# Performance work log

Measured on AMD Instinct MI355X. Metric: run time of the kernel, lower is better.

## Reference

```python
import jax, jax.numpy as jnp
import numpy as np

MAX_DEGREE = 8
N_COEFF = 45  # sum of (2l+1) for l = 0,2,...,8
N_DIRS = 90
BATCH = 50000
N_SHELLS = 4
OUT_SIZE = 4


def _make_ls(max_degree, n_coeff):
    ls = np.zeros(n_coeff, dtype=np.int32)
    for l in range(0, max_degree + 1, 2):
        for m in range(-l, l + 1):
            ls[int(0.5 * l * (l + 1) + m)] = l
    return ls

LS = _make_ls(MAX_DEGREE, N_COEFF)
SCALE = np.sqrt(np.pi / (2.0 * LS + 1.0)).astype(np.float32)  # [K]
LS_IDX = (LS // 2).astype(np.int32)  # [K], index into degree axis of weights


def setup_inputs() -> dict:
    key = jax.random.key(0)
    ks = jax.random.split(key, 10)
    inp = {
        'x': jax.random.normal(ks[0], (BATCH, N_SHELLS, N_COEFF), dtype=jnp.float32),
        'sft': jax.random.normal(ks[1], (N_COEFF, N_DIRS), dtype=jnp.float32),
        'isft': jax.random.normal(ks[2], (N_DIRS, N_COEFF), dtype=jnp.float32),
        'w1': jax.random.uniform(ks[3], (16, N_SHELLS, MAX_DEGREE // 2 + 1), dtype=jnp.float32),
        'w2': jax.random.uniform(ks[4], (32, 16, MAX_DEGREE // 2 + 1), dtype=jnp.float32),
        'w3': jax.random.uniform(ks[5], (64, 32, MAX_DEGREE // 2 + 1), dtype=jnp.float32),
        'w4': jax.random.uniform(ks[6], (32, 64, MAX_DEGREE // 2 + 1), dtype=jnp.float32),
        'w5': jax.random.uniform(ks[7], (16, 32, MAX_DEGREE // 2 + 1), dtype=jnp.float32),
        'w6': jax.random.uniform(ks[8], (4, 16, MAX_DEGREE // 2 + 1), dtype=jnp.float32),
    }
    return inp


def _sconv(x, w, ls_idx, scale):
    # x: [B, C_in, K]; w: [C_out, C_in, L/2+1]
    w_exp = w[:, :, ls_idx]  # [C_out, C_in, K]
    # out[b,o,k] = scale[k] * sum_c w_exp[o,c,k] * x[b,c,k]
    return jnp.einsum('bck,ock->bok', x, w_exp) * scale[None, None, :]


def _nonlinearity(x, sft, isft):
    # x: [B, C, K] -> signal space [B, C, P] -> relu -> back to SH space
    sig = jnp.einsum('pk,bck->bcp', isft, x)
    return jnp.einsum('kp,bcp->bck', sft, jax.nn.relu(sig))


def reference(x, sft, isft, w1, w2, w3, w4, w5, w6):
    ls_idx = jnp.asarray(LS_IDX)
    scale = jnp.asarray(SCALE)
    for w in (w1, w2, w3, w4, w5, w6):
        x = _sconv(x, w, ls_idx, scale)
        x = _nonlinearity(x, sft, isft)
    return jnp.squeeze(x)
```

## Files before the change

kernel.cpp:

```cpp
#include <hip/hip_runtime.h>

#define NT 512

typedef __attribute__((ext_vector_type(8)))  short bh8;
typedef __attribute__((ext_vector_type(16))) float f16v;
typedef __attribute__((ext_vector_type(4)))  float f4v;

#define FW_H    0
#define FW_L    28672
#define W2A32_H 57344
#define W2A32_L 61952
#define W3B_H   66560
#define W3B_L   71168

#define YHo  0
#define S2o  3072
#define XHo  9216
#define NU   12672

__device__ __forceinline__ unsigned short f2bf(float f) {
  unsigned u = __float_as_uint(f);
  return (unsigned short)((u + 0x7fffu + ((u >> 16) & 1u)) >> 16);
}
__device__ __forceinline__ float bf2f(unsigned short h) {
  return __uint_as_float(((unsigned)h) << 16);
}
__device__ __forceinline__ int lidxf(int k) {
  return (k < 1) ? 0 : (k < 6) ? 1 : (k < 15) ? 2 : (k < 28) ? 3 : 4;
}
__device__ __forceinline__ float scale_from_j(int j) {
  float s = 1.7724539f;
  s = (j == 1) ? 0.79266548f : s;
  s = (j == 2) ? 0.59081795f : s;
  s = (j == 3) ? 0.49159026f : s;
  s = (j >= 4) ? 0.42988324f : s;
  return s;
}
__device__ __forceinline__ float rcp_from_j(int j) {
  float s = 0.56418958f;
  s = (j == 1) ? 1.2615663f : s;
  s = (j == 2) ? 1.6925688f : s;
  s = (j == 3) ? 2.0342144f : s;
  s = (j >= 4) ? 2.3262120f : s;
  return s;
}
__device__ __forceinline__ unsigned rne_adj(float v) {
  const unsigned u = __float_as_uint(v);
  return u + 0x7fffu + ((u >> 16) & 1u);
}
__device__ __forceinline__ void store4h(unsigned short* dh,
                                        float v0, float v1, float v2, float v3) {
  const unsigned a0 = rne_adj(v0), a1 = rne_adj(v1);
  const unsigned a2 = rne_adj(v2), a3 = rne_adj(v3);
  *(uint2*)dh = make_uint2(__builtin_amdgcn_perm(a1, a0, 0x07060302u),
                           __builtin_amdgcn_perm(a3, a2, 0x07060302u));
}

__global__ void scnn_prep(const float* __restrict__ sft, const float* __restrict__ isft,
                          const float* __restrict__ w1, const float* __restrict__ w2,
                          const float* __restrict__ w3, const float* __restrict__ w4,
                          const float* __restrict__ w5, const float* __restrict__ w6,
                          unsigned short* __restrict__ wsu) {
  const int gid = blockIdx.x * NT + threadIdx.x;
  const int gstr = gridDim.x * NT;
  const float* wp[6] = {w1, w2, w3, w4, w5, w6};
  const int CIN[6] = {4, 16, 32, 64, 32, 16};
  const int COUT[6] = {16, 32, 64, 32, 16, 4};
  const int LG[6] = {3, 4, 5, 6, 5, 4};
  const int NST[6] = {2, 3, 5, 10, 5, 3};
  const int NTC[6] = {1, 2, 4, 2, 1, 1};
  const int FOFF[6] = {0, 2, 8, 28, 48, 53};
#pragma unroll
  for (int l = 0; l < 6; ++l) {
    const int cin = CIN[l], cout = COUT[l], lg = LG[l], cinP = 1 << lg;
    const int nst = NST[l];
    const int n = NTC[l] * nst * 512;
    const float* w = wp[l];
    const int base = FOFF[l] * 512;
    for (int i = gid; i < n; i += gstr) {
      const int fid = i >> 9, lane = (i >> 3) & 63, e = i & 7;
      const int nt = fid / nst, st = fid - nt * nst;
      const int o = nt * 16 + (lane & 15);
      const int s = st * 32 + (lane >> 4) * 8 + e;
      const int j = s >> lg, c = s & (cinP - 1);
      float v = 0.f;
      if (o < cout && j < 5 && c < cin) v = w[(o * cin + c) * 5 + j];
      const unsigned short h = f2bf(v);
      wsu[FW_H + base + i] = h;
      wsu[FW_L + base + i] = f2bf(v - bf2f(h));
    }
  }
  for (int i = gid; i < 9 * 512; i += gstr) {
    const int fid = i >> 9, lane = (i >> 3) & 63, e = i & 7;
    const int mt = fid / 3, ks = fid - mt * 3;
    const int p = mt * 32 + (lane & 31);
    const int k = ks * 16 + (lane >> 5) * 8 + e;
    const float v = (p < 90 && k < 45) ? isft[p * 45 + k] : 0.f;
    const unsigned short h = f2bf(v);
    wsu[W2A32_H + i] = h;
    wsu[W2A32_L + i] = f2bf(v - bf2f(h));
  }
  for (int i = gid; i < 9 * 512; i += gstr) {
    const int fid = i >> 9, lane = (i >> 3) & 63, e = i & 7;
    const int ntK = fid / 3, sl = fid - ntK * 3;
    const int kk = ntK * 16 + (lane & 15);
    const int p = sl * 32 + (lane >> 4) * 8 + e;
    float v = 0.f;
    if (kk < 45 && p < 90) v = sft[kk * 90 + p] * scale_from_j(lidxf(kk));
    const unsigned short h = f2bf(v);
    wsu[W3B_H + i] = h;
    wsu[W3B_L + i] = f2bf(v - bf2f(h));
  }
}

__device__ __forceinline__ f16v s2tile_pre(const unsigned short* U,
                                           const unsigned short* fh, int nt, int lof,
                                           bh8 pah) {
  f16v a;
#pragma unroll
  for (int e = 0; e < 16; ++e) a[e] = 0.f;
  const unsigned short* yb = U + YHo + nt * 3 * 512 + lof;
  {
    const bh8 bhv = *(const bh8*)&yb[0];
    a = __builtin_amdgcn_mfma_f32_32x32x16_bf16(pah, bhv, a, 0, 0, 0);
  }
#pragma unroll
  for (int ks = 1; ks < 3; ++ks) {
    const bh8 ah = *(const bh8*)&fh[ks * 512];
    const bh8 bhv = *(const bh8*)&yb[ks * 512];
    a = __builtin_amdgcn_mfma_f32_32x32x16_bf16(ah, bhv, a, 0, 0, 0);
  }
  return a;
}
__device__ __forceinline__ void writes_s(unsigned short* U, f16v acc, int mt,
                                         int nt, int llo, int lhi) {
  const int so = S2o + ((nt * 2 + (llo >> 4)) * 3 + mt) * 512 + (llo & 15) * 8 + lhi * 4;
#pragma unroll
  for (int g = 0; g < 4; ++g) {
    store4h(&U[so + g * 128],
            fmaxf(acc[g * 4 + 0], 0.f), fmaxf(acc[g * 4 + 1], 0.f),
            fmaxf(acc[g * 4 + 2], 0.f), fmaxf(acc[g * 4 + 3], 0.f));
  }
}

template <int layer, int mt>
__device__ __forceinline__ void atile(unsigned short* U,
                                      const unsigned short* __restrict__ wsu,
                                      int nt, int l15, int q4, int lof) {
  constexpr int lg   = (layer == 0) ? 3 : (layer == 1) ? 4 : (layer == 2) ? 5
                     : (layer == 3) ? 6 : (layer == 4) ? 5 : 4;
  constexpr int cinP = 1 << lg;
  constexpr int NSTc = (layer == 0) ? 2 : (layer == 1) ? 3 : (layer == 2) ? 5
                     : (layer == 3) ? 10 : (layer == 4) ? 5 : 3;
  constexpr int FOFFc= (layer == 0) ? 0 : (layer == 1) ? 2 : (layer == 2) ? 8
                     : (layer == 3) ? 28 : (layer == 4) ? 48 : 53;
  constexpr int hi5 = (5 * cinP + 31) >> 5;
  constexpr int hi4 = (4 * cinP + 31) >> 5;
  constexpr int lo3 = (3 * cinP) >> 5;
  constexpr int lo4 = cinP >> 3;
  constexpr int lo = (mt == 0) ? 0 : (mt == 1) ? lo3 : lo4;
  constexpr int hi = (mt == 0) ? hi4 : hi5;
  (void)cinP;

  const int k = mt * 16 + l15;
  const int jb = lidxf(k) << lg;
  const unsigned short* wfh = wsu + FW_H + (FOFFc + nt * NSTc) * 512 + lof;
  f4v a;
  a[0] = a[1] = a[2] = a[3] = 0.f;
#pragma unroll
  for (int st = lo; st < hi; ++st) {
    const int S = st * 32 + q4 * 8;
    const unsigned c0 = (unsigned)(S - jb);
    const unsigned cc = c0 < 64u ? c0 : 64u;
    const bh8 xh = *(const bh8*)&U[XHo + k * 72 + (int)cc];
    const bh8 wh = *(const bh8*)&wfh[st * 512];
    a = __builtin_amdgcn_mfma_f32_16x16x32_bf16(xh, wh, a, 0, 0, 0);
  }
  const int off = (((nt >> 1) * 3 + mt) << 9) +
                  ((q4 >> 1) * 32 + (nt & 1) * 16 + l15) * 8 + (q4 & 1) * 4;
  store4h(&U[YHo + off], a[0], a[1], a[2], a[3]);
}

__device__ __forceinline__ void dstore(unsigned short* U, f4v a, int ntK, int mtO,
                                       int l15, int q4, int layer_zero_mode) {
  const int kk = ntK * 16 + l15;
  const int oc = mtO * 16 + q4 * 4;
  store4h(&U[XHo + kk * 72 + oc], a[0], a[1], a[2], a[3]);
  if (layer_zero_mode == 1) {
    *(uint2*)&U[XHo + kk * 72 + oc + 32] = make_uint2(0u, 0u);
  }
  if (layer_zero_mode == 2) {
    *(uint2*)&U[XHo + kk * 72 + oc + 16] = make_uint2(0u, 0u);
  }
}

template <int layer>
__device__ __forceinline__ void layer_body(unsigned short* U,
                                           const unsigned short* __restrict__ wsu,
                                           int tid, int wv, int llo, int lhi,
                                           int l15, int q4, int lof) {
  constexpr int nt16 = (layer == 2) ? 4 : (layer == 1 || layer == 3) ? 2 : 1;
  constexpr int n32  = (layer == 2) ? 2 : 1;
  constexpr int zmode = (layer == 3) ? 1 : (layer == 4) ? 2 : 0;

  {
    constexpr int T = 3 * nt16;
    for (int t = wv; t < T; t += 8) {
      const int mt = t % 3, nt = t / 3;
      if (mt == 0)      atile<layer, 0>(U, wsu, nt, l15, q4, lof);
      else if (mt == 1) atile<layer, 1>(U, wsu, nt, l15, q4, lof);
      else              atile<layer, 2>(U, wsu, nt, l15, q4, lof);
    }
  }
  constexpr int T2 = 3 * n32;
  const bool hA = wv < T2;
  const unsigned short* fh = wsu + W2A32_H + (wv % 3) * 3 * 512 + lof;
  bh8 pah;
  if (hA) pah = *(const bh8*)&fh[0];
  __syncthreads();

  {
    f16v a0;
    if (hA) a0 = s2tile_pre(U, fh, wv / 3, lof, pah);
    if (hA) writes_s(U, a0, wv % 3, wv / 3, llo, lhi);
  }
  const int grp = wv >> 2, mtO = wv & 3;
  const bool hD = mtO < nt16;
  const int ntKa = (grp == 0) ? 0 : 2;
  const unsigned short* fba = wsu + W3B_H + ntKa * 3 * 512 + lof;
  bh8 pb;
  if (hD) pb = *(const bh8*)&fba[0];
  __syncthreads();

  if (hD) {
    const unsigned short* ab = U + S2o + mtO * 3 * 512 + lof;
    if (grp == 0) {
      const unsigned short* fbb = wsu + W3B_H + 3 * 512 + lof;
      f4v a0, a1;
      a0[0] = a0[1] = a0[2] = a0[3] = 0.f;
      a1[0] = a1[1] = a1[2] = a1[3] = 0.f;
#pragma unroll
      for (int sl = 0; sl < 3; ++sl) {
        const bh8 ah = *(const bh8*)&ab[sl * 512];
        bh8 b0h;
        if (sl == 0) b0h = pb;
        else         b0h = *(const bh8*)&fba[sl * 512];
        const bh8 b1h = *(const bh8*)&fbb[sl * 512];
        a0 = __builtin_amdgcn_mfma_f32_16x16x32_bf16(ah, b0h, a0, 0, 0, 0);
        a1 = __builtin_amdgcn_mfma_f32_16x16x32_bf16(ah, b1h, a1, 0, 0, 0);
      }
      dstore(U, a0, 0, mtO, l15, q4, zmode);
      dstore(U, a1, 1, mtO, l15, q4, zmode);
    } else {
      f4v a;
      a[0] = a[1] = a[2] = a[3] = 0.f;
#pragma unroll
      for (int sl = 0; sl < 3; ++sl) {
        const bh8 ah = *(const bh8*)&ab[sl * 512];
        bh8 bh_;
        if (sl == 0) bh_ = pb;
        else         bh_ = *(const bh8*)&fba[sl * 512];
        a = __builtin_amdgcn_mfma_f32_16x16x32_bf16(ah, bh_, a, 0, 0, 0);
      }
      dstore(U, a, 2, mtO, l15, q4, zmode);
    }
  }
  __syncthreads();
}

__global__ __launch_bounds__(NT, 8)
void scnn_main(const float* __restrict__ xin, const unsigned short* __restrict__ wsu,
               float* __restrict__ out) {
  __shared__ __align__(16) unsigned short U[NU];
  const int tid = threadIdx.x, b = blockIdx.x;
  const int lane = tid & 63, wv = tid >> 6;
  const int llo = lane & 31, lhi = lane >> 5;
  const int l15 = lane & 15, q4 = lane >> 4;
  const int lof = lane << 3;

  for (int i = tid; i < 864; i += NT)
    ((uint2*)&U[XHo])[i] = make_uint2(0u, 0u);
  __syncthreads();
  for (int i = tid; i < 180; i += NT) {
    const int c = i / 45, k = i - c * 45;
    const float v = xin[(size_t)b * 180 + i] * scale_from_j(lidxf(k));
    U[XHo + k * 72 + c] = f2bf(v);
  }
  __syncthreads();

  layer_body<0>(U, wsu, tid, wv, llo, lhi, l15, q4, lof);
  layer_body<1>(U, wsu, tid, wv, llo, lhi, l15, q4, lof);
  layer_body<2>(U, wsu, tid, wv, llo, lhi, l15, q4, lof);
  layer_body<3>(U, wsu, tid, wv, llo, lhi, l15, q4, lof);
  layer_body<4>(U, wsu, tid, wv, llo, lhi, l15, q4, lof);
  layer_body<5>(U, wsu, tid, wv, llo, lhi, l15, q4, lof);

  for (int i = tid; i < 180; i += NT) {
    const int c = i / 45, k = i - c * 45;
    const float v = bf2f(U[XHo + k * 72 + c]);
    out[(size_t)b * 180 + i] = v * rcp_from_j(lidxf(k));
  }
}

extern "C" void kernel_launch(void* const* d_in, const int* in_sizes, int n_in,
                              void* d_out, int out_size, void* d_ws, size_t ws_size,
                              hipStream_t stream) {
  (void)n_in; (void)out_size; (void)ws_size;
  const float* x    = (const float*)d_in[0];
  const float* sft  = (const float*)d_in[1];
  const float* isft = (const float*)d_in[2];
  const float* w1   = (const float*)d_in[3];
  const float* w2   = (const float*)d_in[4];
  const float* w3   = (const float*)d_in[5];
  const float* w4   = (const float*)d_in[6];
  const float* w5   = (const float*)d_in[7];
  const float* w6   = (const float*)d_in[8];
  float* out = (float*)d_out;
  unsigned short* wsu = (unsigned short*)d_ws;
  const int nb = in_sizes[0] / 180;
  scnn_prep<<<64, NT, 0, stream>>>(sft, isft, w1, w2, w3, w4, w5, w6, wsu);
  scnn_main<<<nb, NT, 0, stream>>>(x, wsu, out);
}
```

Before: 650.7 us.

## Halve block to four waves and loop tiles over waves per stage

Shrinks the per-sample block from 8 to 4 wavefronts and replaces the fixed wave-to-tile mapping with strided loops over tiles in each stage, dropping the prefetched first operand. Launch bounds change to target 6 blocks per CU, and the prep grid doubles to keep its thread count. The aim is to cut idle waves and barrier cost per sample and fit more blocks per CU, at the cost of serialising more tiles per wave and losing the early weight prefetch.

```diff
diff --git a/kernel.cpp b/kernel.cpp
--- a/kernel.cpp
+++ b/kernel.cpp
@@ -1,6 +1,6 @@
 #include <hip/hip_runtime.h>
 
-#define NT 512
+#define NT 256
 
 typedef __attribute__((ext_vector_type(8)))  short bh8;
 typedef __attribute__((ext_vector_type(16))) float f16v;
@@ -113,19 +113,16 @@
   }
 }
 
-__device__ __forceinline__ f16v s2tile_pre(const unsigned short* U,
-                                           const unsigned short* fh, int nt, int lof,
-                                           bh8 pah) {
+__device__ __forceinline__ f16v s2tile(const unsigned short* U,
+                                       const unsigned short* __restrict__ wsu,
+                                       int mt, int nt, int lof) {
   f16v a;
 #pragma unroll
   for (int e = 0; e < 16; ++e) a[e] = 0.f;
+  const unsigned short* fh = wsu + W2A32_H + mt * 3 * 512 + lof;
   const unsigned short* yb = U + YHo + nt * 3 * 512 + lof;
-  {
-    const bh8 bhv = *(const bh8*)&yb[0];
-    a = __builtin_amdgcn_mfma_f32_32x32x16_bf16(pah, bhv, a, 0, 0, 0);
-  }
-#pragma unroll
-  for (int ks = 1; ks < 3; ++ks) {
+#pragma unroll
+  for (int ks = 0; ks < 3; ++ks) {
     const bh8 ah = *(const bh8*)&fh[ks * 512];
     const bh8 bhv = *(const bh8*)&yb[ks * 512];
     a = __builtin_amdgcn_mfma_f32_32x32x16_bf16(ah, bhv, a, 0, 0, 0);
@@ -205,70 +202,46 @@
 
   {
     constexpr int T = 3 * nt16;
-    for (int t = wv; t < T; t += 8) {
+    for (int t = wv; t < T; t += 4) {
       const int mt = t % 3, nt = t / 3;
       if (mt == 0)      atile<layer, 0>(U, wsu, nt, l15, q4, lof);
       else if (mt == 1) atile<layer, 1>(U, wsu, nt, l15, q4, lof);
       else              atile<layer, 2>(U, wsu, nt, l15, q4, lof);
     }
   }
-  constexpr int T2 = 3 * n32;
-  const bool hA = wv < T2;
-  const unsigned short* fh = wsu + W2A32_H + (wv % 3) * 3 * 512 + lof;
-  bh8 pah;
-  if (hA) pah = *(const bh8*)&fh[0];
   __syncthreads();
 
   {
-    f16v a0;
-    if (hA) a0 = s2tile_pre(U, fh, wv / 3, lof, pah);
-    if (hA) writes_s(U, a0, wv % 3, wv / 3, llo, lhi);
-  }
-  const int grp = wv >> 2, mtO = wv & 3;
-  const bool hD = mtO < nt16;
-  const int ntKa = (grp == 0) ? 0 : 2;
-  const unsigned short* fba = wsu + W3B_H + ntKa * 3 * 512 + lof;
-  bh8 pb;
-  if (hD) pb = *(const bh8*)&fba[0];
-  __syncthreads();
-
-  if (hD) {
-    const unsigned short* ab = U + S2o + mtO * 3 * 512 + lof;
-    if (grp == 0) {
-      const unsigned short* fbb = wsu + W3B_H + 3 * 512 + lof;
-      f4v a0, a1;
-      a0[0] = a0[1] = a0[2] = a0[3] = 0.f;
-      a1[0] = a1[1] = a1[2] = a1[3] = 0.f;
+    constexpr int T2 = 3 * n32;
+    for (int t = wv; t < T2; t += 4) {
+      const int mt = t % 3, nt = t / 3;
+      const f16v a0 = s2tile(U, wsu, mt, nt, lof);
+      writes_s(U, a0, mt, nt, llo, lhi);
+    }
+  }
+  __syncthreads();
+
+  {
+    constexpr int T3 = 3 * nt16;
+    for (int t = wv; t < T3; t += 4) {
+      const int ntK = t % 3, mtO = t / 3;
+      const unsigned short* fb = wsu + W3B_H + ntK * 3 * 512 + lof;
+      const unsigned short* ab = U + S2o + mtO * 3 * 512 + lof;
+      f4v a;
+      a[0] = a[1] = a[2] = a[3] = 0.f;
 #pragma unroll
       for (int sl = 0; sl < 3; ++sl) {
         const bh8 ah = *(const bh8*)&ab[sl * 512];
-        bh8 b0h;
-        if (sl == 0) b0h = pb;
-        else         b0h = *(const bh8*)&fba[sl * 512];
-        const bh8 b1h = *(const bh8*)&fbb[sl * 512];
-        a0 = __builtin_amdgcn_mfma_f32_16x16x32_bf16(ah, b0h, a0, 0, 0, 0);
-        a1 = __builtin_amdgcn_mfma_f32_16x16x32_bf16(ah, b1h, a1, 0, 0, 0);
-      }
-      dstore(U, a0, 0, mtO, l15, q4, zmode);
-      dstore(U, a1, 1, mtO, l15, q4, zmode);
-    } else {
-      f4v a;
-      a[0] = a[1] = a[2] = a[3] = 0.f;
-#pragma unroll
-      for (int sl = 0; sl < 3; ++sl) {
-        const bh8 ah = *(const bh8*)&ab[sl * 512];
-        bh8 bh_;
-        if (sl == 0) bh_ = pb;
-        else         bh_ = *(const bh8*)&fba[sl * 512];
+        const bh8 bh_ = *(const bh8*)&fb[sl * 512];
         a = __builtin_amdgcn_mfma_f32_16x16x32_bf16(ah, bh_, a, 0, 0, 0);
       }
-      dstore(U, a, 2, mtO, l15, q4, zmode);
-    }
-  }
-  __syncthreads();
-}
-
-__global__ __launch_bounds__(NT, 8)
+      dstore(U, a, ntK, mtO, l15, q4, zmode);
+    }
+  }
+  __syncthreads();
+}
+
+__global__ __launch_bounds__(NT, 6)
 void scnn_main(const float* __restrict__ xin, const unsigned short* __restrict__ wsu,
                float* __restrict__ out) {
   __shared__ __align__(16) unsigned short U[NU];
@@ -318,6 +291,6 @@
   float* out = (float*)d_out;
   unsigned short* wsu = (unsigned short*)d_ws;
   const int nb = in_sizes[0] / 180;
-  scnn_prep<<<64, NT, 0, stream>>>(sft, isft, w1, w2, w3, w4, w5, w6, wsu);
+  scnn_prep<<<128, NT, 0, stream>>>(sft, isft, w1, w2, w3, w4, w5, w6, wsu);
   scnn_main<<<nb, NT, 0, stream>>>(x, wsu, out);
 }
```

After: 611.6 us. 1.06x faster.
